# Kernel optimization log

Measured on AMD Instinct MI355X. Metric: run time of the kernel, lower is better.

Reference implementation:

```python
import jax, jax.numpy as jnp
import numpy as np

HEADS = 6
WSIZE = 8
SHIFTS = 4
EPS = 1e-5


def conv1x1(x, w, b=None):
    # x: (B,C,H,W), w: (O,C)
    y = jnp.einsum('bchw,oc->bohw', x, w)
    if b is not None:
        y = y + b[None, :, None, None]
    return y


def spatial_shift(x):
    # ShiftConv2d1 depthwise fixed-kernel conv == per-group spatial shift with zero pad
    C = x.shape[1]
    g = C // 5
    x0, x1, x2, x3, x4 = (x[:, :g], x[:, g:2 * g], x[:, 2 * g:3 * g],
                          x[:, 3 * g:4 * g], x[:, 4 * g:])
    left = jnp.pad(x0[:, :, :, 1:], ((0, 0), (0, 0), (0, 0), (0, 1)))   # kernel (1,2)
    right = jnp.pad(x1[:, :, :, :-1], ((0, 0), (0, 0), (0, 0), (1, 0)))  # kernel (1,0)
    up = jnp.pad(x2[:, :, 1:, :], ((0, 0), (0, 0), (0, 1), (0, 0)))      # kernel (2,1)
    down = jnp.pad(x3[:, :, :-1, :], ((0, 0), (0, 0), (1, 0), (0, 0)))   # kernel (0,1)
    return jnp.concatenate([left, right, up, down, x4], axis=1)


def window_attn(xb, ws, heads, shifts):
    # xb: (B, 2*heads*c, H, W); self-similarity attention q@q^T (no separate K, no scaling)
    if shifts > 0:
        xb = jnp.roll(xb, (-(ws // 2), -(ws // 2)), axis=(2, 3))
    b, c2, H, W = xb.shape
    cd = c2 // (2 * heads)
    nh, nw = H // ws, W // ws
    t = xb.reshape(b, 2, heads, cd, nh, ws, nw, ws)
    t = t.transpose(1, 0, 4, 6, 2, 5, 7, 3).reshape(2, b * nh * nw, heads, ws * ws, cd)
    q, v = t[0], t[1]
    atn = jax.nn.softmax(jnp.einsum('whnc,whmc->whnm', q, q), axis=-1)
    o = jnp.einsum('whnm,whmc->whnc', atn, v)
    o = o.reshape(b, nh, nw, heads, ws, ws, cd)
    o = o.transpose(0, 3, 6, 1, 4, 2, 5).reshape(b, heads * cd, H, W)
    if shifts > 0:
        o = jnp.roll(o, (ws // 2, ws // 2), axis=(2, 3))
    return o


def setup_inputs() -> dict:
    key = jax.random.key(0)
    ks = jax.random.split(key, 8)
    B, C, H, W = 2, 180, 256, 256
    s = 0.05
    return {
        'x': jax.random.normal(ks[0], (B, C, H, W), jnp.float32),
        'w0': jax.random.normal(ks[1], (2 * C, C), jnp.float32) * s,
        'b0': jnp.zeros((2 * C,), jnp.float32),
        'w1': jax.random.normal(ks[2], (C, 2 * C), jnp.float32) * s,
        'b1': jnp.zeros((C,), jnp.float32),
        'w_in': jax.random.normal(ks[3], (2 * C, C), jnp.float32) * s,
        'b_in': jnp.zeros((2 * C,), jnp.float32),
        'bn_g': jnp.ones((2 * C,), jnp.float32),
        'bn_b': jnp.zeros((2 * C,), jnp.float32),
        'w_out': jax.random.normal(ks[4], (C, C), jnp.float32) * s,
        'b_out': jnp.zeros((C,), jnp.float32),
    }


def reference(x, w0, b0, w1, b1, w_in, b_in, bn_g, bn_b, w_out, b_out):
    # --- LFE (shift-conv FFN), exp_ratio=2, relu ---
    y = conv1x1(spatial_shift(x), w0, b0)
    y = jax.nn.relu(y)
    y = conv1x1(spatial_shift(y), w1, b1)
    x = y + x
    # --- GMSA (3 parallel shifted-window self-similarity attentions) ---
    z = conv1x1(x, w_in, b_in)
    mu = z.mean(axis=(0, 2, 3), keepdims=True)
    var = z.var(axis=(0, 2, 3), keepdims=True)  # biased, matching BN training forward
    z = (z - mu) / jnp.sqrt(var + EPS) * bn_g[None, :, None, None] + bn_b[None, :, None, None]
    cs = z.shape[1] // 3
    sizes = [WSIZE // 4, WSIZE // 2, WSIZE]
    outs = [window_attn(z[:, i * cs:(i + 1) * cs], sizes[i], HEADS, SHIFTS)
            for i in range(3)]
    out = conv1x1(jnp.concatenate(outs, axis=1), w_out, b_out)
    return out + x
```

## Files before the change

kernel.cpp:

```cpp
#include <hip/hip_runtime.h>
#include <hip/hip_bf16.h>

#define HWSZ 65536
#define NPIX 131072

typedef unsigned short u16;
typedef __bf16 bf16x8 __attribute__((ext_vector_type(8)));
typedef float f32x4 __attribute__((ext_vector_type(4)));
typedef unsigned short u16x2 __attribute__((ext_vector_type(2)));
typedef unsigned short u16x4 __attribute__((ext_vector_type(4)));
typedef unsigned short u16x8 __attribute__((ext_vector_type(8)));

__device__ inline u16 f2bf(float f) {
    unsigned int x = __builtin_bit_cast(unsigned int, f);
    unsigned int r = x + 0x7FFFu + ((x >> 16) & 1u);
    return (u16)(r >> 16);
}
__device__ inline float bf2f(u16 u) {
    unsigned int x = ((unsigned int)u) << 16;
    return __builtin_bit_cast(float, x);
}

__global__ __launch_bounds__(256) void prep_w(
    const float* __restrict__ w0, const float* __restrict__ w1,
    const float* __restrict__ wi, const float* __restrict__ wo,
    u16* __restrict__ W0p, u16* __restrict__ W1p,
    u16* __restrict__ Wip, u16* __restrict__ Wop)
{
    const int i = blockIdx.x * 256 + threadIdx.x;
    {
        const int r = i / 192, c = i % 192;
        const bool ok = (r < 360) && (c < 180);
        W0p[i] = ok ? f2bf(w0[r * 180 + c]) : (u16)0;
        Wip[i] = ok ? f2bf(wi[r * 180 + c]) : (u16)0;
    }
    {
        const int r = i / 384, c = i % 384;
        W1p[i] = (r < 180 && c < 360) ? f2bf(w1[r * 360 + c]) : (u16)0;
    }
    if (i < 36864) {
        const int r = i / 192, c = i % 192;
        Wop[i] = (r < 180 && c < 180) ? f2bf(wo[r * 180 + c]) : (u16)0;
    }
}

template<int CI, int CO, int G, int INM, int XSTR, bool RELU, int RES, int OUTM, int OSTR, bool COSPLIT>
__global__ __launch_bounds__(256, 4) void conv_v9(
    const void* __restrict__ Xv, const u16* __restrict__ Wp,
    const float* __restrict__ bias, const void* __restrict__ Rv,
    void* __restrict__ Yv)
{
    constexpr int CI_PAD = ((CI + 31) / 32) * 32;
    constexpr int NSTEP  = CI_PAD / 32;
    constexpr int LDK    = 40;

    __shared__ u16 Xt[2][64 * LDK];

    const int tid = threadIdx.x;
    const int bid = blockIdx.x;
    int px_tile, co0;
    if (COSPLIT) {
        co0     = ((bid >> 3) & 1) * 192;
        px_tile = ((bid >> 4) << 3) | (bid & 7);
    } else {
        co0 = 0; px_tile = bid;
    }
    const int p0   = px_tile << 6;
    const int b    = p0 >> 16;
    const int pix0 = p0 & 65535;
    const int h    = pix0 >> 8;
    const int w0c  = pix0 & 255;
    const int lane = tid & 63, wid = tid >> 6;
    const int lr = lane & 15, lg = lane >> 4;
    const int co_wave = co0 + wid * 48;

    const float* Xf = (const float*)Xv + (size_t)b * CI * HWSZ;
    const u16*   Xh = (const u16*)Xv;

    const int xn  = tid & 63;
    const int k4a = tid >> 6;

    auto loadX = [&](int kt, u16x4 (&r)[2]) {
        #pragma unroll
        for (int it = 0; it < 2; ++it) {
            const int k4 = k4a + it * 4;
            const int c0 = kt + k4 * 4;
            u16x4 v = {0, 0, 0, 0};
            if (c0 < CI) {
                int dh = 0, dw = 0;
                if (G > 0) {
                    const int g = c0 / G;
                    if      (g == 0) dw = 1;
                    else if (g == 1) dw = -1;
                    else if (g == 2) dh = 1;
                    else if (g == 3) dh = -1;
                }
                const int hh = h + dh;
                const int wp = w0c + xn + dw;
                if (hh >= 0 && hh < 256 && wp >= 0 && wp < 256) {
                    if constexpr (INM == 1) {
                        v = *(const u16x4*)&Xh[(size_t)((b << 16) | (hh << 8) | wp) * XSTR + c0];
                    } else {
                        const float* xs = Xf + (size_t)c0 * HWSZ + hh * 256 + wp;
                        #pragma unroll
                        for (int j = 0; j < 4; ++j) v[j] = f2bf(xs[(size_t)j * HWSZ]);
                    }
                }
            }
            r[it] = v;
        }
    };

    auto loadW = [&](int kt, bf16x8 (&a)[3]) {
        #pragma unroll
        for (int mf = 0; mf < 3; ++mf)
            a[mf] = *(const bf16x8*)&Wp[(size_t)(co_wave + mf * 16 + lr) * CI_PAD + kt + lg * 8];
    };

    auto writeLDS = [&](u16x4 (&r)[2], int buf) {
        *(u16x4*)&Xt[buf][xn * LDK + k4a * 4]       = r[0];
        *(u16x4*)&Xt[buf][xn * LDK + (k4a + 4) * 4] = r[1];
    };

    f32x4 acc[3][4] = {};
    u16x4 raw[2][2];
    bf16x8 af[2][3];

    loadX(0, raw[0]);
    loadW(0, af[0]);
    writeLDS(raw[0], 0);

    #pragma unroll
    for (int s = 0; s < NSTEP; ++s) {
        const int cur = s & 1, nxt = cur ^ 1;
        __syncthreads();
        if (s + 1 < NSTEP) {
            loadX((s + 1) * 32, raw[nxt]);
            loadW((s + 1) * 32, af[nxt]);
        }
        bf16x8 bfr[4];
        #pragma unroll
        for (int nf = 0; nf < 4; ++nf)
            bfr[nf] = *(const bf16x8*)&Xt[cur][(nf * 16 + lr) * LDK + lg * 8];
        #pragma unroll
        for (int mf = 0; mf < 3; ++mf)
            #pragma unroll
            for (int nf = 0; nf < 4; ++nf)
                acc[mf][nf] = __builtin_amdgcn_mfma_f32_16x16x32_bf16(
                    af[cur][mf], bfr[nf], acc[mf][nf], 0, 0, 0);
        if (s + 1 < NSTEP) writeLDS(raw[nxt], nxt);
    }

    const float* Rf = (const float*)Rv;
    const u16*   Rh = (const u16*)Rv;
    #pragma unroll
    for (int mf = 0; mf < 3; ++mf) {
        const int co_b = co_wave + mf * 16 + lg * 4;
        if (co_b >= CO) continue;
        #pragma unroll
        for (int nf = 0; nf < 4; ++nf) {
            const int pl = pix0 + nf * 16 + lr;
            const size_t pg = (size_t)p0 + nf * 16 + lr;
            float v[4];
            #pragma unroll
            for (int r = 0; r < 4; ++r) {
                v[r] = acc[mf][nf][r] + bias[co_b + r];
                if (RELU) v[r] = fmaxf(v[r], 0.f);
            }
            if (RES == 1) {
                #pragma unroll
                for (int r = 0; r < 4; ++r)
                    v[r] += Rf[((size_t)(b * CO + co_b + r)) * HWSZ + pl];
            }
            if (RES == 2) {
                u16x4 rr = *(const u16x4*)&Rh[pg * 180 + co_b];
                #pragma unroll
                for (int r = 0; r < 4; ++r) v[r] += bf2f(rr[r]);
            }
            if (OUTM == 1) {
                u16x4 o;
                #pragma unroll
                for (int r = 0; r < 4; ++r) o[r] = f2bf(v[r]);
                *(u16x4*)&((u16*)Yv)[pg * OSTR + co_b] = o;
            } else {
                #pragma unroll
                for (int r = 0; r < 4; ++r)
                    ((float*)Yv)[((size_t)(b * CO + co_b + r)) * HWSZ + pl] = v[r];
            }
        }
    }
}

template<int CI, int CO, int G, int XSTR, bool RELU, int RES, int OUTM, int OSTR, bool COSPLIT>
__global__ __launch_bounds__(256) void conv_v10(
    const u16* __restrict__ Xh, const u16* __restrict__ Wp,
    const float* __restrict__ bias, const void* __restrict__ Rv,
    void* __restrict__ Yv)
{
    constexpr int CI_PAD = ((CI + 31) / 32) * 32;
    constexpr int NSTEP  = CI_PAD / 32;

    __shared__ u16 Xt[2][256 * 8];

    const int tid = threadIdx.x;
    const int bid = blockIdx.x;
    int px_tile, co0;
    if (COSPLIT) {
        co0     = ((bid >> 3) & 1) * 192;
        px_tile = ((bid >> 4) << 3) | (bid & 7);
    } else {
        co0 = 0; px_tile = bid;
    }
    const int p0   = px_tile << 6;
    const int b    = p0 >> 16;
    const int pix0 = p0 & 65535;
    const int h    = pix0 >> 8;
    const int w0c  = pix0 & 255;
    const int lane = tid & 63, wid = tid >> 6;
    const int lr = lane & 15, lg = lane >> 4;
    const int co_wave = co0 + wid * 48;

    const int sg  = (wid << 6) | lane;
    const int spx = sg >> 2;
    const int khp = sg & 3;
    const int kh  = khp ^ ((spx >> 1) & 3);

    auto stage = [&](int kt, int buf) {
        const int c0 = kt + kh * 8;
        u16* ldst_lane = &Xt[buf][sg * 8];
        int dh = 0, dw = 0; bool uni = true;
        if (G > 0) {
            const int g0 = c0 / G;
            uni = (g0 == (c0 + 7) / G);
            if      (g0 == 0) dw = 1;
            else if (g0 == 1) dw = -1;
            else if (g0 == 2) dh = 1;
            else if (g0 == 3) dh = -1;
        }
        const int hh = h + dh, wp = w0c + spx + dw;
        const bool pxok = (hh >= 0 && hh < 256 && wp >= 0 && wp < 256);
        if (c0 < CI && uni && pxok) {
            const u16* src = &Xh[(size_t)((b << 16) | (hh << 8) | wp) * XSTR + c0];
            u16* wbase = &Xt[buf][(wid << 6) * 8];
            __builtin_amdgcn_global_load_lds(
                (const __attribute__((address_space(1))) unsigned int*)src,
                (__attribute__((address_space(3))) unsigned int*)wbase, 16, 0, 0);
        } else {
            u16x8 t = {0, 0, 0, 0, 0, 0, 0, 0};
            if (c0 < CI && pxok) {
                #pragma unroll
                for (int j = 0; j < 8; ++j) {
                    const int c = c0 + j;
                    if (c < CI) {
                        int dh2 = 0, dw2 = 0;
                        if (G > 0) {
                            const int g = c / G;
                            if      (g == 0) dw2 = 1;
                            else if (g == 1) dw2 = -1;
                            else if (g == 2) dh2 = 1;
                            else if (g == 3) dh2 = -1;
                        }
                        const int h2 = h + dh2, w2 = w0c + spx + dw2;
                        if (h2 >= 0 && h2 < 256 && w2 >= 0 && w2 < 256)
                            t[j] = Xh[(size_t)((b << 16) | (h2 << 8) | w2) * XSTR + c];
                    }
                }
            }
            *(u16x8*)ldst_lane = t;
        }
    };

    auto loadW = [&](int kt, bf16x8 (&a)[3]) {
        #pragma unroll
        for (int mf = 0; mf < 3; ++mf)
            a[mf] = *(const bf16x8*)&Wp[(size_t)(co_wave + mf * 16 + lr) * CI_PAD + kt + lg * 8];
    };

    f32x4 acc[3][4] = {};
    bf16x8 af[2][3];

    stage(0, 0);
    loadW(0, af[0]);
    __syncthreads();

    #pragma unroll
    for (int s = 0; s < NSTEP; ++s) {
        const int cur = s & 1, nxt = cur ^ 1;
        if (s + 1 < NSTEP) {
            stage((s + 1) * 32, nxt);
            loadW((s + 1) * 32, af[nxt]);
        }
        bf16x8 bfr[4];
        #pragma unroll
        for (int nf = 0; nf < 4; ++nf) {
            const int pxr = nf * 16 + lr;
            const int kpp = lg ^ ((pxr >> 1) & 3);
            bfr[nf] = *(const bf16x8*)&Xt[cur][pxr * 32 + kpp * 8];
        }
        #pragma unroll
        for (int mf = 0; mf < 3; ++mf)
            #pragma unroll
            for (int nf = 0; nf < 4; ++nf)
                acc[mf][nf] = __builtin_amdgcn_mfma_f32_16x16x32_bf16(
                    af[cur][mf], bfr[nf], acc[mf][nf], 0, 0, 0);
        __syncthreads();
    }

    const float* Rf = (const float*)Rv;
    const u16*   Rh = (const u16*)Rv;
    #pragma unroll
    for (int mf = 0; mf < 3; ++mf) {
        const int co_b = co_wave + mf * 16 + lg * 4;
        if (co_b >= CO) continue;
        #pragma unroll
        for (int nf = 0; nf < 4; ++nf) {
            const int pl = pix0 + nf * 16 + lr;
            const size_t pg = (size_t)p0 + nf * 16 + lr;
            float v[4];
            #pragma unroll
            for (int r = 0; r < 4; ++r) {
                v[r] = acc[mf][nf][r] + bias[co_b + r];
                if (RELU) v[r] = fmaxf(v[r], 0.f);
            }
            if (RES == 1) {
                #pragma unroll
                for (int r = 0; r < 4; ++r)
                    v[r] += Rf[((size_t)(b * CO + co_b + r)) * HWSZ + pl];
            }
            if (RES == 2) {
                u16x4 rr = *(const u16x4*)&Rh[pg * 180 + co_b];
                #pragma unroll
                for (int r = 0; r < 4; ++r) v[r] += bf2f(rr[r]);
            }
            if (OUTM == 1) {
                u16x4 o;
                #pragma unroll
                for (int r = 0; r < 4; ++r) o[r] = f2bf(v[r]);
                *(u16x4*)&((u16*)Yv)[pg * OSTR + co_b] = o;
            } else {
                #pragma unroll
                for (int r = 0; r < 4; ++r)
                    ((float*)Yv)[((size_t)(b * CO + co_b + r)) * HWSZ + pl] = v[r];
            }
        }
    }
}

__global__ __launch_bounds__(256) void bn_part(const u16* __restrict__ zt,
                                               float* __restrict__ part)
{
    const int tid = threadIdx.x;
    const int oc  = tid & 63;
    const int pp  = tid >> 6;
    if (oc >= 45) return;
    const int stripe = blockIdx.x * 4 + pp;
    const int pb = blockIdx.x * 1024 + pp;
    float s[8] = {}, q[8] = {};
    for (int i = 0; i < 256; ++i) {
        const int p = pb + i * 4;
        u16x8 t = *(const u16x8*)&zt[(size_t)p * 360 + oc * 8];
        #pragma unroll
        for (int j = 0; j < 8; ++j) {
            float v = bf2f(t[j]);
            s[j] += v; q[j] += v * v;
        }
    }
    float* pr = part + ((size_t)stripe * 45 + oc) * 16;
    #pragma unroll
    for (int j = 0; j < 8; ++j) { pr[j] = s[j]; pr[8 + j] = q[j]; }
}

__global__ __launch_bounds__(256) void bn_fin(const float* __restrict__ part,
                                              const float* __restrict__ g,
                                              const float* __restrict__ bb,
                                              float* __restrict__ sc,
                                              float* __restrict__ sh)
{
    const int oc = blockIdx.x;
    const int t  = threadIdx.x;
    const float* p1 = part + ((size_t)t * 45 + oc) * 16;
    const float* p2 = part + ((size_t)(t + 256) * 45 + oc) * 16;
    float v[16];
    #pragma unroll
    for (int k = 0; k < 16; ++k) v[k] = p1[k] + p2[k];
    #pragma unroll
    for (int k = 0; k < 16; ++k)
        for (int m = 32; m; m >>= 1) v[k] += __shfl_xor(v[k], m, 64);
    __shared__ float red[4][16];
    if ((t & 63) == 0) {
        #pragma unroll
        for (int k = 0; k < 16; ++k) red[t >> 6][k] = v[k];
    }
    __syncthreads();
    if (t == 0) {
        const float invN = 1.f / (float)NPIX;
        #pragma unroll
        for (int j = 0; j < 8; ++j) {
            const int c = oc * 8 + j;
            float su = red[0][j] + red[1][j] + red[2][j] + red[3][j];
            float sq = red[0][8+j] + red[1][8+j] + red[2][8+j] + red[3][8+j];
            float mean = su * invN;
            float var  = sq * invN - mean * mean;
            float istd = 1.f / sqrtf(var + 1e-5f);
            float s = g[c] * istd;
            sc[c] = s;
            sh[c] = bb[c] - mean * s;
        }
    }
}

template<int WS>
__global__ __launch_bounds__(256) void attn_v2(
    const u16* __restrict__ zt, const float* __restrict__ scale,
    const float* __restrict__ shiftc, u16* __restrict__ ot, int chunk)
{
    constexpr int NP  = WS * WS;
    constexpr int GPB = 256 / NP;
    constexpr int SH  = WS / 2;
    constexpr int NW  = 256 / WS;

    __shared__ float qs[256 * 12];
    __shared__ float vs[256 * 12];

    const int tid = threadIdx.x;
    const int lg  = tid / NP;
    const int n   = tid % NP;
    const int gidx = blockIdx.x * GPB + lg;

    const int head = gidx % 6;
    const int win  = gidx / 6;
    const int wcol = win % NW;
    const int tmp  = win / NW;
    const int wrow = tmp % NW;
    const int b    = tmp / NW;

    const int i = n / WS, j = n % WS;
    const int hh = (wrow * WS + i + SH) & 255;
    const int ww = (wcol * WS + j + SH) & 255;
    const size_t zrow = (size_t)((b << 16) | (hh << 8) | ww) * 360;

    const int cq = chunk * 120 + head * 10;
    const int cv = cq + 60;

    float q[10];
    float* qrow = &qs[tid * 12];
    float* vrow = &vs[tid * 12];
    #pragma unroll
    for (int c2 = 0; c2 < 5; ++c2) {
        u16x2 uq = *(const u16x2*)&zt[zrow + cq + c2 * 2];
        u16x2 uv = *(const u16x2*)&zt[zrow + cv + c2 * 2];
        float q0 = bf2f(uq[0]) * scale[cq + c2 * 2]     + shiftc[cq + c2 * 2];
        float q1 = bf2f(uq[1]) * scale[cq + c2 * 2 + 1] + shiftc[cq + c2 * 2 + 1];
        float v0 = bf2f(uv[0]) * scale[cv + c2 * 2]     + shiftc[cv + c2 * 2];
        float v1 = bf2f(uv[1]) * scale[cv + c2 * 2 + 1] + shiftc[cv + c2 * 2 + 1];
        q[c2 * 2] = q0; q[c2 * 2 + 1] = q1;
        qrow[c2 * 2] = q0; qrow[c2 * 2 + 1] = q1;
        vrow[c2 * 2] = v0; vrow[c2 * 2 + 1] = v1;
    }
    qrow[10] = 0.f; qrow[11] = 0.f;
    vrow[10] = 0.f; vrow[11] = 0.f;
    __syncthreads();

    const float* qg = &qs[(lg * NP) * 12];
    const float* vg = &vs[(lg * NP) * 12];

    float mx = -1e30f;
    for (int m = 0; m < NP; ++m) {
        f32x4 a0 = *(const f32x4*)&qg[m * 12];
        f32x4 a1 = *(const f32x4*)&qg[m * 12 + 4];
        f32x4 a2 = *(const f32x4*)&qg[m * 12 + 8];
        float d = q[0]*a0[0] + q[1]*a0[1] + q[2]*a0[2] + q[3]*a0[3]
                + q[4]*a1[0] + q[5]*a1[1] + q[6]*a1[2] + q[7]*a1[3]
                + q[8]*a2[0] + q[9]*a2[1];
        mx = fmaxf(mx, d);
    }
    float s = 0.f;
    float o[10] = {};
    for (int m = 0; m < NP; ++m) {
        f32x4 a0 = *(const f32x4*)&qg[m * 12];
        f32x4 a1 = *(const f32x4*)&qg[m * 12 + 4];
        f32x4 a2 = *(const f32x4*)&qg[m * 12 + 8];
        float d = q[0]*a0[0] + q[1]*a0[1] + q[2]*a0[2] + q[3]*a0[3]
                + q[4]*a1[0] + q[5]*a1[1] + q[6]*a1[2] + q[7]*a1[3]
                + q[8]*a2[0] + q[9]*a2[1];
        float e = __expf(d - mx);
        s += e;
        f32x4 b0 = *(const f32x4*)&vg[m * 12];
        f32x4 b1 = *(const f32x4*)&vg[m * 12 + 4];
        f32x4 b2 = *(const f32x4*)&vg[m * 12 + 8];
        o[0] += e * b0[0]; o[1] += e * b0[1]; o[2] += e * b0[2]; o[3] += e * b0[3];
        o[4] += e * b1[0]; o[5] += e * b1[1]; o[6] += e * b1[2]; o[7] += e * b1[3];
        o[8] += e * b2[0]; o[9] += e * b2[1];
    }
    const float inv = 1.f / s;
    u16* orow = ot + (size_t)((b << 16) | (hh << 8) | ww) * 180 + chunk * 60 + head * 10;
    #pragma unroll
    for (int c2 = 0; c2 < 5; ++c2) {
        u16x2 ov;
        ov[0] = f2bf(o[c2 * 2] * inv);
        ov[1] = f2bf(o[c2 * 2 + 1] * inv);
        *(u16x2*)&orow[c2 * 2] = ov;
    }
}

extern "C" void kernel_launch(void* const* d_in, const int* in_sizes, int n_in,
                              void* d_out, int out_size, void* d_ws, size_t ws_size,
                              hipStream_t stream)
{
    const float* x     = (const float*)d_in[0];
    const float* w0    = (const float*)d_in[1];
    const float* b0    = (const float*)d_in[2];
    const float* w1    = (const float*)d_in[3];
    const float* b1    = (const float*)d_in[4];
    const float* w_in  = (const float*)d_in[5];
    const float* b_in  = (const float*)d_in[6];
    const float* bn_g  = (const float*)d_in[7];
    const float* bn_b  = (const float*)d_in[8];
    const float* w_out = (const float*)d_in[9];
    const float* b_out = (const float*)d_in[10];
    float* out = (float*)d_out;

    u16* y   = (u16*)d_ws;
    u16* x1b = y   + (size_t)NPIX * 360;
    u16* ot  = x1b + (size_t)NPIX * 180;
    u16* W0p = ot  + (size_t)NPIX * 180;
    u16* Wip = W0p + 384 * 192;
    u16* W1p = Wip + 384 * 192;
    u16* Wop = W1p + 192 * 384;
    float* part   = (float*)(Wop + 192 * 192);
    float* scale  = part + 512 * 45 * 16;
    float* shiftc = scale + 360;
    u16* zt = y;

    dim3 blk(256);

    prep_w<<<dim3(288), blk, 0, stream>>>(w0, w1, w_in, w_out, W0p, W1p, Wip, Wop);

    conv_v9<180, 360, 36, 0, 0,   true,  0, 1, 360, true>
        <<<dim3(4096), blk, 0, stream>>>(x, W0p, b0, nullptr, y);
    conv_v10<360, 180, 72, 360, false, 1, 1, 180, false>
        <<<dim3(2048), blk, 0, stream>>>(y, W1p, b1, x, x1b);
    conv_v10<180, 360, 0,  180, false, 0, 1, 360, true>
        <<<dim3(4096), blk, 0, stream>>>(x1b, Wip, b_in, nullptr, zt);
    bn_part<<<dim3(128), blk, 0, stream>>>(zt, part);
    bn_fin<<<dim3(45), blk, 0, stream>>>(part, bn_g, bn_b, scale, shiftc);
    attn_v2<2><<<dim3(3072), blk, 0, stream>>>(zt, scale, shiftc, ot, 0);
    attn_v2<4><<<dim3(3072), blk, 0, stream>>>(zt, scale, shiftc, ot, 1);
    attn_v2<8><<<dim3(3072), blk, 0, stream>>>(zt, scale, shiftc, ot, 2);
    conv_v10<180, 180, 0,  180, false, 2, 0, 0, false>
        <<<dim3(2048), blk, 0, stream>>>(ot, Wop, b_out, x1b, out);
}
```

Measured before the change: 410.1 us.

## Load activation MFMA fragments directly from global memory, dropping LDS staging

The 1x1 conv kernel used to stage activation tiles into LDS with global_load_lds and swizzling, then read B fragments back from LDS behind a barrier each K step. It now loads each lane's B fragment straight from global memory into registers, double-buffered, and handles the shifted channel groups with per-lane offsets and a two-load merge at group boundaries. This removes LDS traffic and __syncthreads. In exchange, each wave issues its own global loads (the four waves re-read the same pixels), loads may be unaligned, and register pressure rises.

```diff
diff --git a/kernel.cpp b/kernel.cpp
--- a/kernel.cpp
+++ b/kernel.cpp
@@ -10,6 +10,7 @@
 typedef unsigned short u16x2 __attribute__((ext_vector_type(2)));
 typedef unsigned short u16x4 __attribute__((ext_vector_type(4)));
 typedef unsigned short u16x8 __attribute__((ext_vector_type(8)));
+typedef unsigned short u16x8u __attribute__((ext_vector_type(8), aligned(4)));
 
 __device__ inline u16 f2bf(float f) {
     unsigned int x = __builtin_bit_cast(unsigned int, f);
@@ -192,15 +193,13 @@
 }
 
 template<int CI, int CO, int G, int XSTR, bool RELU, int RES, int OUTM, int OSTR, bool COSPLIT>
-__global__ __launch_bounds__(256) void conv_v10(
+__global__ __launch_bounds__(256) void conv_v12(
     const u16* __restrict__ Xh, const u16* __restrict__ Wp,
     const float* __restrict__ bias, const void* __restrict__ Rv,
     void* __restrict__ Yv)
 {
     constexpr int CI_PAD = ((CI + 31) / 32) * 32;
     constexpr int NSTEP  = CI_PAD / 32;
-
-    __shared__ u16 Xt[2][256 * 8];
 
     const int tid = threadIdx.x;
     const int bid = blockIdx.x;
@@ -214,96 +213,77 @@
     const int p0   = px_tile << 6;
     const int b    = p0 >> 16;
     const int pix0 = p0 & 65535;
-    const int h    = pix0 >> 8;
-    const int w0c  = pix0 & 255;
     const int lane = tid & 63, wid = tid >> 6;
     const int lr = lane & 15, lg = lane >> 4;
     const int co_wave = co0 + wid * 48;
 
-    const int sg  = (wid << 6) | lane;
-    const int spx = sg >> 2;
-    const int khp = sg & 3;
-    const int kh  = khp ^ ((spx >> 1) & 3);
-
-    auto stage = [&](int kt, int buf) {
-        const int c0 = kt + kh * 8;
-        u16* ldst_lane = &Xt[buf][sg * 8];
-        int dh = 0, dw = 0; bool uni = true;
-        if (G > 0) {
-            const int g0 = c0 / G;
-            uni = (g0 == (c0 + 7) / G);
-            if      (g0 == 0) dw = 1;
-            else if (g0 == 1) dw = -1;
-            else if (g0 == 2) dh = 1;
-            else if (g0 == 3) dh = -1;
-        }
-        const int hh = h + dh, wp = w0c + spx + dw;
-        const bool pxok = (hh >= 0 && hh < 256 && wp >= 0 && wp < 256);
-        if (c0 < CI && uni && pxok) {
-            const u16* src = &Xh[(size_t)((b << 16) | (hh << 8) | wp) * XSTR + c0];
-            u16* wbase = &Xt[buf][(wid << 6) * 8];
-            __builtin_amdgcn_global_load_lds(
-                (const __attribute__((address_space(1))) unsigned int*)src,
-                (__attribute__((address_space(3))) unsigned int*)wbase, 16, 0, 0);
-        } else {
-            u16x8 t = {0, 0, 0, 0, 0, 0, 0, 0};
-            if (c0 < CI && pxok) {
-                #pragma unroll
-                for (int j = 0; j < 8; ++j) {
-                    const int c = c0 + j;
-                    if (c < CI) {
-                        int dh2 = 0, dw2 = 0;
-                        if (G > 0) {
-                            const int g = c / G;
-                            if      (g == 0) dw2 = 1;
-                            else if (g == 1) dw2 = -1;
-                            else if (g == 2) dh2 = 1;
-                            else if (g == 3) dh2 = -1;
-                        }
-                        const int h2 = h + dh2, w2 = w0c + spx + dw2;
-                        if (h2 >= 0 && h2 < 256 && w2 >= 0 && w2 < 256)
-                            t[j] = Xh[(size_t)((b << 16) | (h2 << 8) | w2) * XSTR + c];
-                    }
+    int hhv[4], wpv[4];
+    long pbase[4];
+    #pragma unroll
+    for (int nf = 0; nf < 4; ++nf) {
+        const int pix = pix0 + nf * 16 + lr;
+        hhv[nf] = pix >> 8; wpv[nf] = pix & 255;
+        pbase[nf] = (long)((b << 16) | pix) * XSTR;
+    }
+
+    auto shiftOf = [&](int g, int nf, int& off, bool& ok) {
+        off = 0; ok = true;
+        if      (g == 0) { off =  XSTR;        ok = (wpv[nf] < 255); }
+        else if (g == 1) { off = -XSTR;        ok = (wpv[nf] > 0);   }
+        else if (g == 2) { off =  (XSTR << 8); ok = (hhv[nf] < 255); }
+        else if (g == 3) { off = -(XSTR << 8); ok = (hhv[nf] > 0);   }
+    };
+    auto loadv = [&](long idx) -> u16x8 {
+        return __builtin_bit_cast(u16x8, *(const u16x8u*)&Xh[idx]);
+    };
+
+    auto loadFrags = [&](int s, bf16x8 (&bfr)[4], bf16x8 (&af)[3]) {
+        const int c0 = s * 32 + lg * 8;
+        #pragma unroll
+        for (int nf = 0; nf < 4; ++nf) {
+            u16x8 a = {0, 0, 0, 0, 0, 0, 0, 0};
+            if constexpr (G > 0) {
+                const int g0 = (c0 < CI) ? (c0 / G) : 4;
+                int off0; bool ok0;
+                shiftOf(g0, nf, off0, ok0);
+                if (ok0) a = loadv(pbase[nf] + off0 + c0);
+                const int ce = (c0 + 7 < CI) ? (c0 + 7) : (CI - 1);
+                const int g1 = (c0 < CI) ? (ce / G) : 4;
+                if (g1 != g0) {
+                    int off1; bool ok1;
+                    shiftOf(g1, nf, off1, ok1);
+                    u16x8 b2 = {0, 0, 0, 0, 0, 0, 0, 0};
+                    if (ok1) b2 = loadv(pbase[nf] + off1 + c0);
+                    const int Bb = g1 * G;
+                    #pragma unroll
+                    for (int j = 0; j < 8; ++j)
+                        if (c0 + j >= Bb) a[j] = b2[j];
                 }
-            }
-            *(u16x8*)ldst_lane = t;
-        }
+            } else {
+                a = loadv(pbase[nf] + c0);
+            }
+            bfr[nf] = __builtin_bit_cast(bf16x8, a);
+        }
+        #pragma unroll
+        for (int mf = 0; mf < 3; ++mf)
+            af[mf] = *(const bf16x8*)&Wp[(size_t)(co_wave + mf * 16 + lr) * CI_PAD + c0];
     };
 
-    auto loadW = [&](int kt, bf16x8 (&a)[3]) {
-        #pragma unroll
-        for (int mf = 0; mf < 3; ++mf)
-            a[mf] = *(const bf16x8*)&Wp[(size_t)(co_wave + mf * 16 + lr) * CI_PAD + kt + lg * 8];
-    };
-
     f32x4 acc[3][4] = {};
-    bf16x8 af[2][3];
-
-    stage(0, 0);
-    loadW(0, af[0]);
-    __syncthreads();
+    bf16x8 bfr[2][4], af[2][3];
+
+    loadFrags(0, bfr[0], af[0]);
 
     #pragma unroll
     for (int s = 0; s < NSTEP; ++s) {
         const int cur = s & 1, nxt = cur ^ 1;
-        if (s + 1 < NSTEP) {
-            stage((s + 1) * 32, nxt);
-            loadW((s + 1) * 32, af[nxt]);
-        }
-        bf16x8 bfr[4];
-        #pragma unroll
-        for (int nf = 0; nf < 4; ++nf) {
-            const int pxr = nf * 16 + lr;
-            const int kpp = lg ^ ((pxr >> 1) & 3);
-            bfr[nf] = *(const bf16x8*)&Xt[cur][pxr * 32 + kpp * 8];
-        }
+        if (s + 1 < NSTEP) loadFrags(s + 1, bfr[nxt], af[nxt]);
         #pragma unroll
         for (int mf = 0; mf < 3; ++mf)
             #pragma unroll
             for (int nf = 0; nf < 4; ++nf)
                 acc[mf][nf] = __builtin_amdgcn_mfma_f32_16x16x32_bf16(
-                    af[cur][mf], bfr[nf], acc[mf][nf], 0, 0, 0);
-        __syncthreads();
+                    af[cur][mf], bfr[cur][nf], acc[mf][nf], 0, 0, 0);
     }
 
     const float* Rf = (const float*)Rv;
@@ -538,15 +518,15 @@
 
     conv_v9<180, 360, 36, 0, 0,   true,  0, 1, 360, true>
         <<<dim3(4096), blk, 0, stream>>>(x, W0p, b0, nullptr, y);
-    conv_v10<360, 180, 72, 360, false, 1, 1, 180, false>
+    conv_v12<360, 180, 72, 360, false, 1, 1, 180, false>
         <<<dim3(2048), blk, 0, stream>>>(y, W1p, b1, x, x1b);
-    conv_v10<180, 360, 0,  180, false, 0, 1, 360, true>
+    conv_v12<180, 360, 0,  180, false, 0, 1, 360, true>
         <<<dim3(4096), blk, 0, stream>>>(x1b, Wip, b_in, nullptr, zt);
     bn_part<<<dim3(128), blk, 0, stream>>>(zt, part);
     bn_fin<<<dim3(45), blk, 0, stream>>>(part, bn_g, bn_b, scale, shiftc);
     attn_v2<2><<<dim3(3072), blk, 0, stream>>>(zt, scale, shiftc, ot, 0);
     attn_v2<4><<<dim3(3072), blk, 0, stream>>>(zt, scale, shiftc, ot, 1);
     attn_v2<8><<<dim3(3072), blk, 0, stream>>>(zt, scale, shiftc, ot, 2);
-    conv_v10<180, 180, 0,  180, false, 2, 0, 0, false>
+    conv_v12<180, 180, 0,  180, false, 2, 0, 0, false>
         <<<dim3(2048), blk, 0, stream>>>(ot, Wop, b_out, x1b, out);
 }
```

After: 427.4 us. 4.2% more time.
